# Kernel optimization log

Hardware: AMD Instinct MI355X
Metric: run time of the kernel (lower is better)

## Reference

```python
import jax, jax.numpy as jnp
import numpy as np
import math

H = 8  # num_heads

def _gelu(x):
    return jax.nn.gelu(x, approximate=False)

def setup_inputs() -> dict:
    key = jax.random.key(0)
    ks = jax.random.split(key, 16)
    B, N, T, D = 2, 16, 127, 128
    s = 0.02
    inp = {}
    inp["padded_batches"] = jax.random.normal(ks[0], (B, N, T, D), jnp.float32)
    inp["masks"] = jax.random.randint(ks[1], (B, N, T), 0, 2).astype(jnp.int32)
    inp["positions_3d"] = jax.random.normal(ks[2], (B, N, T, 3), jnp.float32)
    inp["Wq"] = jax.random.normal(ks[3], (D, D), jnp.float32) * s
    inp["bq"] = jnp.zeros((D,), jnp.float32)
    inp["Wk"] = jax.random.normal(ks[4], (D, D), jnp.float32) * s
    inp["bk"] = jnp.zeros((D,), jnp.float32)
    inp["Wv"] = jax.random.normal(ks[5], (D, D), jnp.float32) * s
    inp["bv"] = jnp.zeros((D,), jnp.float32)
    inp["gamma"] = jnp.ones((D,), jnp.float32)
    inp["beta"] = jnp.zeros((D,), jnp.float32)
    inp["token_embedding"] = jax.random.normal(ks[6], (1, D), jnp.float32)
    inp["Wb1"] = jax.random.normal(ks[7], (6, 64), jnp.float32) * s
    inp["bb1"] = jnp.zeros((64,), jnp.float32)
    inp["Wb2"] = jax.random.normal(ks[8], (64, H), jnp.float32) * s
    inp["bb2"] = jnp.zeros((H,), jnp.float32)
    inp["Wv1"] = jax.random.normal(ks[9], (6, 128), jnp.float32) * s
    inp["bv1"] = jnp.zeros((128,), jnp.float32)
    inp["Wv2"] = jax.random.normal(ks[10], (128, D), jnp.float32) * s
    inp["bv2"] = jnp.zeros((D,), jnp.float32)
    return inp

def reference(padded_batches, masks, positions_3d, Wq, bq, Wk, bk, Wv, bv, gamma, beta, token_embedding, Wb1, bb1, Wb2, bb2, Wv1, bv1, Wv2, bv2):
    B, N, T, D = padded_batches.shape
    Hd = D // H
    L = T + 1
    scale = 1.0 / math.sqrt(Hd)
    # prepend cls token
    cls = jnp.broadcast_to(token_embedding, (B, N, 1, D))
    x = jnp.concatenate([cls, padded_batches], axis=-2)  # [B,N,L,D]
    q = (x @ Wq + bq).reshape(B * N, L, H, Hd).transpose(0, 2, 1, 3)
    k = (x @ Wk + bk).reshape(B * N, L, H, Hd).transpose(0, 2, 1, 3)
    v = (x @ Wv + bv).reshape(B * N, L, H, Hd).transpose(0, 2, 1, 3)
    keep = jnp.concatenate([jnp.ones((B, N, 1), masks.dtype), masks], axis=-1)
    large_neg = jnp.finfo(jnp.float32).min
    key_mask = jnp.where(keep == 0, large_neg, 0.0).astype(jnp.float32).reshape(B * N, 1, 1, L)
    logits = jnp.einsum('bhid,bhjd->bhij', q, k) * scale
    # relative positional features
    pos = jnp.concatenate([jnp.zeros((B, N, 1, 3), positions_3d.dtype), positions_3d], axis=-2).reshape(B * N, L, 3)
    diff = pos[:, :, None, :] - pos[:, None, :, :]  # [BN,L,L,3]
    dist2 = jnp.sum(diff ** 2, axis=-1, keepdims=True)
    dist = jnp.sqrt(dist2)
    rel_feat = jnp.concatenate([diff, dist, dist, dist2], axis=-1)  # [BN,L,L,6]
    rel_bias = (_gelu(rel_feat @ Wb1 + bb1) @ Wb2 + bb2).transpose(0, 3, 1, 2)  # [BN,H,L,L]
    rel_bias = rel_bias.at[:, :, 0, :].set(0.0).at[:, :, :, 0].set(0.0)
    logits = logits + rel_bias + key_mask
    w = jax.nn.softmax(logits, axis=-1)
    attn = jnp.einsum('bhij,bhjd->bhid', w, v)
    rel_val = (_gelu(rel_feat @ Wv1 + bv1) @ Wv2 + bv2).reshape(B * N, L, L, H, Hd).transpose(0, 3, 1, 2, 4)
    rel_val = rel_val.at[:, :, 0, :, :].set(0.0).at[:, :, :, 0, :].set(0.0)
    attn = attn + jnp.einsum('bhij,bhijc->bhic', w, rel_val)
    attn = attn.transpose(0, 2, 1, 3).reshape(B, N, L, D)
    st = attn[:, :, :1, :] + x[:, :, :1, :]
    mu = jnp.mean(st, axis=-1, keepdims=True)
    var = jnp.var(st, axis=-1, keepdims=True)
    sum_token = (st - mu) / jnp.sqrt(var + 1e-5) * gamma + beta
    out = attn[:, :, 1:, :] + x[:, :, 1:, :]
    return (out, sum_token)
```

## Files before the change

kernel.cpp:

```cpp
#include <hip/hip_runtime.h>
#include <hip/hip_bf16.h>
#include <math.h>

#define BN 32
#define L 128
#define D 128
#define TT 127
#define NH 8

typedef float f32x4 __attribute__((ext_vector_type(4)));
typedef short s16x8 __attribute__((ext_vector_type(8)));

__device__ __forceinline__ float gelu_sig(float x) {
    float e = __expf(-1.702f * x);
    return x * __builtin_amdgcn_rcpf(1.0f + e);
}
__device__ __forceinline__ unsigned short f2bf(float f) {
    unsigned u = __float_as_uint(f);
    return (unsigned short)((u + 0x7fffu + ((u >> 16) & 1u)) >> 16);
}
__device__ __forceinline__ float bf2f(unsigned short v) {
    return __uint_as_float((unsigned)v << 16);
}

__global__ __launch_bounds__(256)
void qkv_bias_kernel(const float* __restrict__ padded, const float* __restrict__ tok,
                     const float* __restrict__ Wq, const float* __restrict__ bq,
                     const float* __restrict__ Wk, const float* __restrict__ bk,
                     const float* __restrict__ Wv, const float* __restrict__ bv,
                     const float* __restrict__ Wb1, const float* __restrict__ bb1,
                     const float* __restrict__ Wb2, const float* __restrict__ bb2,
                     const float* __restrict__ Wv1, const float* __restrict__ bv1,
                     const float* __restrict__ Wv2,
                     const int* __restrict__ masks, const float* __restrict__ pos3d,
                     float* __restrict__ Qo, float* __restrict__ Ko,
                     unsigned short* __restrict__ VF,
                     float* __restrict__ RVW, unsigned short* __restrict__ WV2F,
                     unsigned short* __restrict__ BIAS) {
    const int bid = blockIdx.x;
    const int tid = threadIdx.x;

    if (bid < 384) {
        const int chunk = bid / 96;
        const int rem = bid % 96;
        const int mat = rem >> 5;
        const int s = rem & 31;
        const float* W = (mat == 0) ? Wq : (mat == 1) ? Wk : Wv;
        const float* bias = (mat == 0) ? bq : (mat == 1) ? bk : bv;
        float* outp = (mat == 0) ? Qo : Ko;

        __shared__ unsigned short Xs[32][136];
        {
            const int row = tid >> 3;
            const int colbase = (tid & 7) * 16;
            const int i = chunk * 32 + row;
            const float* src = (i == 0) ? tok : &padded[(size_t)s * TT * D + (size_t)(i - 1) * D];
#pragma unroll
            for (int k4 = 0; k4 < 4; ++k4) {
                float4 v = *(const float4*)&src[colbase + k4 * 4];
                unsigned lo = (unsigned)f2bf(v.x) | ((unsigned)f2bf(v.y) << 16);
                unsigned hi = (unsigned)f2bf(v.z) | ((unsigned)f2bf(v.w) << 16);
                *(uint2*)&Xs[row][colbase + k4 * 4] = make_uint2(lo, hi);
            }
        }
        __syncthreads();

        const int wave = tid >> 6;
        const int lane = tid & 63;
        const int hA = lane & 15;
        const int kg = lane >> 4;

        s16x8 afr[2][4];
#pragma unroll
        for (int m = 0; m < 2; ++m)
#pragma unroll
            for (int kt = 0; kt < 4; ++kt)
                afr[m][kt] = *(const s16x8*)&Xs[m * 16 + hA][kt * 32 + kg * 8];

        f32x4 acc[2][2];
#pragma unroll
        for (int m = 0; m < 2; ++m)
#pragma unroll
            for (int n = 0; n < 2; ++n) acc[m][n] = (f32x4){0.f, 0.f, 0.f, 0.f};

#pragma unroll
        for (int kt = 0; kt < 4; ++kt) {
#pragma unroll
            for (int n = 0; n < 2; ++n) {
                const int col = (2 * wave + n) * 16 + hA;
                s16x8 bw;
#pragma unroll
                for (int e = 0; e < 8; ++e)
                    bw[e] = (short)f2bf(W[(size_t)(kt * 32 + kg * 8 + e) * D + col]);
                acc[0][n] = __builtin_amdgcn_mfma_f32_16x16x32_bf16(afr[0][kt], bw, acc[0][n], 0, 0, 0);
                acc[1][n] = __builtin_amdgcn_mfma_f32_16x16x32_bf16(afr[1][kt], bw, acc[1][n], 0, 0, 0);
            }
        }

        if (mat != 2) {
#pragma unroll
            for (int n = 0; n < 2; ++n) {
                const int col = (2 * wave + n) * 16 + hA;
                const float bc = bias[col];
#pragma unroll
                for (int m = 0; m < 2; ++m)
#pragma unroll
                    for (int r = 0; r < 4; ++r) {
                        const int row = chunk * 32 + m * 16 + kg * 4 + r;
                        outp[(size_t)s * L * D + (size_t)row * D + col] = acc[m][n][r] + bc;
                    }
            }
        } else {
            __syncthreads();
#pragma unroll
            for (int n = 0; n < 2; ++n) {
                const int col = (2 * wave + n) * 16 + hA;
                const float bc = bias[col];
#pragma unroll
                for (int m = 0; m < 2; ++m)
#pragma unroll
                    for (int r = 0; r < 4; ++r)
                        Xs[m * 16 + kg * 4 + r][col] = f2bf(acc[m][n][r] + bc);
            }
            __syncthreads();
#pragma unroll
            for (int pass = 0; pass < 2; ++pass) {
                const int idx = pass * 256 + tid;
                const int fl = idx >> 6, ln = idx & 63;
                unsigned short v8[8];
#pragma unroll
                for (int e = 0; e < 8; ++e)
                    v8[e] = Xs[(ln >> 4) * 8 + e][fl * 16 + (ln & 15)];
                *(uint4*)&VF[(size_t)s * 16384 + ((size_t)(chunk * 8 + fl) * 64 + ln) * 8] = *(uint4*)v8;
            }
        }

        if (bid == 0) {
            if (tid < 128) {
                const int cc = tid;
                RVW[cc * 8 + 0] = Wv1[0 * 128 + cc];
                RVW[cc * 8 + 1] = Wv1[1 * 128 + cc];
                RVW[cc * 8 + 2] = Wv1[2 * 128 + cc];
                RVW[cc * 8 + 3] = Wv1[3 * 128 + cc] + Wv1[4 * 128 + cc];
                RVW[cc * 8 + 4] = Wv1[5 * 128 + cc];
                RVW[cc * 8 + 5] = bv1[cc];
                RVW[cc * 8 + 6] = 0.f;
                RVW[cc * 8 + 7] = 0.f;
            }
            for (int idx = tid; idx < 16384; idx += 256) {
                int f = idx >> 9, r = idx & 511, ln = r >> 3, e = r & 7;
                int kt = f >> 3, ng = f & 7;
                int row = kt * 32 + (ln >> 4) * 8 + e;
                int col = ng * 16 + (ln & 15);
                WV2F[idx] = f2bf(Wv2[(size_t)row * D + col]);
            }
        }
    } else {
        const int b2 = bid - 384;
        const int s = b2 >> 6;
        const int jp = b2 & 63;
        const int wv = tid >> 6;
        const int lane = tid & 63;
        const int j = jp * 2 + (wv >> 1);
        const int i = (wv & 1) * 64 + lane;

        if (j == 0) return;
        if (!masks[(size_t)s * TT + (j - 1)]) return;
        const float* pj = pos3d + ((size_t)s * TT + (j - 1)) * 3;
        const int im1 = (i > 0) ? (i - 1) : 0;
        const float* pi = pos3d + ((size_t)s * TT + im1) * 3;
        const float pix = (i > 0) ? pi[0] : 0.f;
        const float piy = (i > 0) ? pi[1] : 0.f;
        const float piz = (i > 0) ? pi[2] : 0.f;
        const float dx = pix - pj[0], dy = piy - pj[1], dz = piz - pj[2];
        const float dist2 = dx * dx + dy * dy + dz * dz;
        const float dist = sqrtf(dist2);

        float bias[NH];
#pragma unroll
        for (int hh = 0; hh < NH; ++hh) bias[hh] = 0.f;
#pragma unroll 2
        for (int u = 0; u < 64; ++u) {
            const float w0 = Wb1[u];
            const float w1 = Wb1[64 + u];
            const float w2 = Wb1[128 + u];
            const float w3 = Wb1[192 + u] + Wb1[256 + u];
            const float w4 = Wb1[320 + u];
            float hv = bb1[u];
            hv = fmaf(dx, w0, hv);
            hv = fmaf(dy, w1, hv);
            hv = fmaf(dz, w2, hv);
            hv = fmaf(dist, w3, hv);
            hv = fmaf(dist2, w4, hv);
            hv = gelu_sig(hv);
            const float* w2p = &Wb2[u * 8];
            bias[0] = fmaf(hv, w2p[0], bias[0]);
            bias[1] = fmaf(hv, w2p[1], bias[1]);
            bias[2] = fmaf(hv, w2p[2], bias[2]);
            bias[3] = fmaf(hv, w2p[3], bias[3]);
            bias[4] = fmaf(hv, w2p[4], bias[4]);
            bias[5] = fmaf(hv, w2p[5], bias[5]);
            bias[6] = fmaf(hv, w2p[6], bias[6]);
            bias[7] = fmaf(hv, w2p[7], bias[7]);
        }
        if (i > 0) {
            uint4 ow;
            ow.x = (unsigned)f2bf(bias[0] + bb2[0]) | ((unsigned)f2bf(bias[1] + bb2[1]) << 16);
            ow.y = (unsigned)f2bf(bias[2] + bb2[2]) | ((unsigned)f2bf(bias[3] + bb2[3]) << 16);
            ow.z = (unsigned)f2bf(bias[4] + bb2[4]) | ((unsigned)f2bf(bias[5] + bb2[5]) << 16);
            ow.w = (unsigned)f2bf(bias[6] + bb2[6]) | ((unsigned)f2bf(bias[7] + bb2[7]) << 16);
            *(uint4*)&BIAS[(((size_t)s * L + i) * L + j) * 8] = ow;
        }
    }
}

__global__ __launch_bounds__(256)
void logits_kernel(const float* __restrict__ Q, const float* __restrict__ K,
                   __hip_bfloat16* __restrict__ LW) {
    const int s = blockIdx.x >> 3;
    const int h = blockIdx.x & 7;
    const int tid = threadIdx.x;
    const int wv = tid >> 6;
    const int lane = tid & 63;
    const int lrn = lane & 15;
    const int kg = lane >> 4;

    __shared__ float Qs[128][16];
    __shared__ float Ks[128][16];
    for (int e = tid; e < 2048; e += 256) {
        int i = e >> 4, d = e & 15;
        Qs[i][d] = Q[((size_t)s * L + i) * D + h * 16 + d];
        Ks[i][d] = K[((size_t)s * L + i) * D + h * 16 + d];
    }
    __syncthreads();

    s16x8 afr[2];
#pragma unroll
    for (int m = 0; m < 2; ++m) {
        s16x8 a;
#pragma unroll
        for (int e = 0; e < 8; ++e) a[e] = 0;
        if (kg < 2) {
            const int i = wv * 32 + m * 16 + lrn;
            float4 q0 = *(const float4*)&Qs[i][kg * 8];
            float4 q1 = *(const float4*)&Qs[i][kg * 8 + 4];
            a[0] = (short)f2bf(q0.x); a[1] = (short)f2bf(q0.y);
            a[2] = (short)f2bf(q0.z); a[3] = (short)f2bf(q0.w);
            a[4] = (short)f2bf(q1.x); a[5] = (short)f2bf(q1.y);
            a[6] = (short)f2bf(q1.z); a[7] = (short)f2bf(q1.w);
        }
        afr[m] = a;
    }

    __hip_bfloat16* lw = LW + ((size_t)(s * NH + h) * L) * L;
#pragma unroll
    for (int n = 0; n < 8; ++n) {
        s16x8 b;
#pragma unroll
        for (int e = 0; e < 8; ++e) b[e] = 0;
        if (kg < 2) {
            const int j = n * 16 + lrn;
            float4 k0 = *(const float4*)&Ks[j][kg * 8];
            float4 k1 = *(const float4*)&Ks[j][kg * 8 + 4];
            b[0] = (short)f2bf(k0.x); b[1] = (short)f2bf(k0.y);
            b[2] = (short)f2bf(k0.z); b[3] = (short)f2bf(k0.w);
            b[4] = (short)f2bf(k1.x); b[5] = (short)f2bf(k1.y);
            b[6] = (short)f2bf(k1.z); b[7] = (short)f2bf(k1.w);
        }
#pragma unroll
        for (int m = 0; m < 2; ++m) {
            f32x4 acc = (f32x4){0.f, 0.f, 0.f, 0.f};
            acc = __builtin_amdgcn_mfma_f32_16x16x32_bf16(afr[m], b, acc, 0, 0, 0);
#pragma unroll
            for (int r = 0; r < 4; ++r)
                lw[(size_t)(wv * 32 + m * 16 + kg * 4 + r) * L + n * 16 + lrn] =
                    __float2bfloat16(acc[r] * 0.25f);
        }
    }
}

__global__ __launch_bounds__(256, 4)
void attn_kernel(const float* __restrict__ padded, const int* __restrict__ masks,
                 const float* __restrict__ pos3d,
                 const float* __restrict__ gamma, const float* __restrict__ beta,
                 const float* __restrict__ tok,
                 const float* __restrict__ RVW,
                 const unsigned short* __restrict__ WV2F,
                 const float* __restrict__ bv2,
                 const unsigned short* __restrict__ VF, const __hip_bfloat16* __restrict__ LW,
                 const unsigned short* __restrict__ BIAS,
                 float* __restrict__ out) {
    const int i = blockIdx.x;
    const int s = blockIdx.y;
    const int tid = threadIdx.x;
    const int wave = tid >> 6;
    const int lane = tid & 63;
    const int hA = lane & 15;
    const int kg = lane >> 4;
    const int j = tid & 127;
    const int hbase = (tid >> 7) * 4;

    __shared__ float4 feat4_lds[144];
    __shared__ float  feat5_lds[L];
    __shared__ unsigned short w_bf[NH][136];
    __shared__ unsigned short wu_bf[NH][136];
    __shared__ unsigned short gs_bf[NH][136];
    __shared__ float  a12_lds[2][D];
    __shared__ float  reds[4][NH];
    __shared__ float  red2[2][2];
    __shared__ unsigned long long kb_lds[2];
    __shared__ int    jmap_lds[128];

    __hip_bfloat16 lr4[4];
#pragma unroll
    for (int k = 0; k < 4; ++k)
        lr4[k] = LW[((size_t)(s * NH + hbase + k) * L + i) * L + j];
    const int keep = (j == 0) ? 1 : masks[(size_t)s * TT + (j - 1)];
    const int ub = (i > 0) && (j > 0) && keep;
    uint2 braw = make_uint2(0u, 0u);
    if (ub) braw = *(const uint2*)&BIAS[(((size_t)s * L + i) * L + j) * 8 + hbase];

    const unsigned long long bal = __ballot(keep != 0);
    if (lane == 0 && wave < 2) kb_lds[wave] = bal;

    if (tid < 128) {
        float pix = 0.f, piy = 0.f, piz = 0.f;
        if (i > 0) { const float* pp = pos3d + ((size_t)s * TT + (i - 1)) * 3; pix = pp[0]; piy = pp[1]; piz = pp[2]; }
        float pjx = 0.f, pjy = 0.f, pjz = 0.f;
        if (tid > 0) { const float* pp = pos3d + ((size_t)s * TT + (tid - 1)) * 3; pjx = pp[0]; pjy = pp[1]; pjz = pp[2]; }
        const float dx = pix - pjx, dy = piy - pjy, dz = piz - pjz;
        const float dist2 = dx * dx + dy * dy + dz * dz;
        const float dist = sqrtf(dist2);
        feat4_lds[tid + (tid >> 3)] = make_float4(dx, dy, dz, dist);
        feat5_lds[tid] = dist2;
        jmap_lds[tid] = 0;
    }
    for (int idx = tid; idx < NH * 68; idx += 256) {
        ((unsigned*)w_bf)[idx] = 0u;
        ((unsigned*)wu_bf)[idx] = 0u;
    }
    __syncthreads();

    const unsigned long long b0 = kb_lds[0];
    const int nk = __popcll(b0) + __popcll(kb_lds[1]);
    const int NK32 = (nk + 31) >> 5;
    int rank = 0;
    if (keep) {
        rank = __popcll(bal & ((1ull << lane) - 1)) + ((wave & 1) ? __popcll(b0) : 0);
        if (wave < 2) jmap_lds[rank] = j;
    }

    float badd[4];
    badd[0] = bf2f((unsigned short)(braw.x & 0xffffu));
    badd[1] = bf2f((unsigned short)(braw.x >> 16));
    badd[2] = bf2f((unsigned short)(braw.y & 0xffffu));
    badd[3] = bf2f((unsigned short)(braw.y >> 16));
    float p4[4];
#pragma unroll
    for (int k = 0; k < 4; ++k) {
        float lv = __bfloat162float(lr4[k]) + badd[k];
        p4[k] = keep ? __expf(lv) : 0.f;
    }
#pragma unroll
    for (int k = 0; k < 4; ++k) {
        float v = p4[k];
        for (int off = 32; off >= 1; off >>= 1) v += __shfl_xor(v, off, 64);
        if (lane == 0) reds[wave][hbase + k] = v;
    }
    __syncthreads();
    if (keep) {
        const int pb = (tid >> 7) * 2;
#pragma unroll
        for (int k = 0; k < 4; ++k) {
            const int hh = hbase + k;
            float inv = __builtin_amdgcn_rcpf(reds[pb][hh] + reds[pb + 1][hh]);
            unsigned short wn = f2bf(p4[k] * inv);
            w_bf[hh][rank] = wn;
            wu_bf[hh][j] = wn;
        }
    }
    __syncthreads();

    const int ng0 = 2 * wave;
    const unsigned short* VFs = VF + (size_t)s * 16384;

    f32x4 acc1[2];
    acc1[0] = (f32x4){0.f, 0.f, 0.f, 0.f};
    acc1[1] = (f32x4){0.f, 0.f, 0.f, 0.f};
#pragma unroll
    for (int kt = 0; kt < 4; ++kt) {
        s16x8 wuf;
#pragma unroll
        for (int e = 0; e < 8; ++e) wuf[e] = 0;
        if (hA < NH)
            wuf = *(const s16x8*)&wu_bf[hA][kt * 32 + kg * 8];
#pragma unroll
        for (int n = 0; n < 2; ++n) {
            const int f = kt * 8 + ng0 + n;
            s16x8 bw = *(const s16x8*)&VFs[((size_t)f * 64 + lane) * 8];
            acc1[n] = __builtin_amdgcn_mfma_f32_16x16x32_bf16(wuf, bw, acc1[n], 0, 0, 0);
        }
    }
#pragma unroll
    for (int n = 0; n < 2; ++n) {
        const int f = ng0 + n;
        if (kg == (f >> 2)) a12_lds[0][f * 16 + hA] = acc1[n][f & 3];
    }

    if (i > 0) {
        float rvw[2][6];
#pragma unroll
        for (int n = 0; n < 2; ++n) {
            const int c = (ng0 + n) * 16 + hA;
            float4 ra = *(const float4*)&RVW[(size_t)c * 8 + 0];
            rvw[n][0] = ra.x; rvw[n][1] = ra.y; rvw[n][2] = ra.z; rvw[n][3] = ra.w;
            rvw[n][4] = RVW[(size_t)c * 8 + 4];
            rvw[n][5] = RVW[(size_t)c * 8 + 5];
        }

        f32x4 accG[2];
#pragma unroll
        for (int n = 0; n < 2; ++n) accG[n] = (f32x4){0.f, 0.f, 0.f, 0.f};

#pragma unroll
        for (int kt = 0; kt < 4; ++kt) {
            if (kt >= NK32) break;
            s16x8 wf;
#pragma unroll
            for (int e = 0; e < 8; ++e) wf[e] = 0;
            if (hA < NH) {
                wf = *(const s16x8*)&w_bf[hA][kt * 32 + kg * 8];
                if (kt == 0 && kg == 0) wf[0] = 0;
            }
            s16x8 bfr[2];
#pragma unroll
            for (int e = 0; e < 8; ++e) {
                const int jj = jmap_lds[kt * 32 + kg * 8 + e];
                float4 fa = feat4_lds[jj + (jj >> 3)];
                float f5 = feat5_lds[jj];
#pragma unroll
                for (int n = 0; n < 2; ++n) {
                    float hv = rvw[n][5];
                    hv = fmaf(fa.x, rvw[n][0], hv);
                    hv = fmaf(fa.y, rvw[n][1], hv);
                    hv = fmaf(fa.z, rvw[n][2], hv);
                    hv = fmaf(fa.w, rvw[n][3], hv);
                    hv = fmaf(f5,  rvw[n][4], hv);
                    bfr[n][e] = (short)f2bf(gelu_sig(hv));
                }
            }
#pragma unroll
            for (int n = 0; n < 2; ++n)
                accG[n] = __builtin_amdgcn_mfma_f32_16x16x32_bf16(wf, bfr[n], accG[n], 0, 0, 0);
        }

        if (lane < 32) {
#pragma unroll
            for (int n = 0; n < 2; ++n)
#pragma unroll
                for (int r = 0; r < 4; ++r)
                    gs_bf[(lane >> 4) * 4 + r][(ng0 + n) * 16 + hA] = f2bf(accG[n][r]);
        }
        __syncthreads();

        f32x4 acc2[2];
#pragma unroll
        for (int n = 0; n < 2; ++n) acc2[n] = (f32x4){0.f, 0.f, 0.f, 0.f};
#pragma unroll
        for (int kt = 0; kt < 4; ++kt) {
            s16x8 gf;
#pragma unroll
            for (int e = 0; e < 8; ++e) gf[e] = 0;
            if (hA < NH)
                gf = *(const s16x8*)&gs_bf[hA][kt * 32 + kg * 8];
#pragma unroll
            for (int n = 0; n < 2; ++n) {
                const int f = kt * 8 + ng0 + n;
                s16x8 bw = *(const s16x8*)&WV2F[((size_t)f * 64 + lane) * 8];
                acc2[n] = __builtin_amdgcn_mfma_f32_16x16x32_bf16(gf, bw, acc2[n], 0, 0, 0);
            }
        }
#pragma unroll
        for (int n = 0; n < 2; ++n) {
            const int f = ng0 + n;
            if (kg == (f >> 2)) a12_lds[1][f * 16 + hA] = acc2[n][f & 3];
        }
        __syncthreads();

        if (tid < 128) {
            const float S1 = 1.0f - bf2f(wu_bf[tid >> 4][0]);
            const size_t o = (size_t)s * TT * D + (size_t)(i - 1) * D + tid;
            out[o] = a12_lds[0][tid] + a12_lds[1][tid] + S1 * bv2[tid] + padded[o];
        }
    } else {
        __syncthreads();

        float st = 0.f;
        if (tid < 128) {
            st = a12_lds[0][tid] + tok[tid];
            float sum = st, sum2 = st * st;
            for (int off = 32; off >= 1; off >>= 1) {
                sum += __shfl_xor(sum, off, 64);
                sum2 += __shfl_xor(sum2, off, 64);
            }
            if (lane == 0) { red2[wave][0] = sum; red2[wave][1] = sum2; }
        }
        __syncthreads();
        if (tid < 128) {
            float sum = red2[0][0] + red2[1][0];
            float sum2 = red2[0][1] + red2[1][1];
            const float mu = sum * (1.0f / 128.0f);
            const float var = sum2 * (1.0f / 128.0f) - mu * mu;
            const float y = (st - mu) * rsqrtf(var + 1e-5f) * gamma[tid] + beta[tid];
            out[(size_t)BN * TT * D + (size_t)s * D + tid] = y;
        }
    }
}

extern "C" void kernel_launch(void* const* d_in, const int* in_sizes, int n_in,
                              void* d_out, int out_size, void* d_ws, size_t ws_size,
                              hipStream_t stream) {
    const float* padded = (const float*)d_in[0];
    const int*   masks  = (const int*)d_in[1];
    const float* pos3d  = (const float*)d_in[2];
    const float* Wq = (const float*)d_in[3];
    const float* bq = (const float*)d_in[4];
    const float* Wk = (const float*)d_in[5];
    const float* bk = (const float*)d_in[6];
    const float* Wv = (const float*)d_in[7];
    const float* bv = (const float*)d_in[8];
    const float* gamma = (const float*)d_in[9];
    const float* beta  = (const float*)d_in[10];
    const float* tok   = (const float*)d_in[11];
    const float* Wb1 = (const float*)d_in[12];
    const float* bb1 = (const float*)d_in[13];
    const float* Wb2 = (const float*)d_in[14];
    const float* bb2 = (const float*)d_in[15];
    const float* Wv1 = (const float*)d_in[16];
    const float* bv1 = (const float*)d_in[17];
    const float* Wv2 = (const float*)d_in[18];
    const float* bv2 = (const float*)d_in[19];
    float* out = (float*)d_out;

    float* Q  = (float*)d_ws;
    float* K  = Q + (size_t)BN * L * D;
    unsigned short* VF = (unsigned short*)(K + (size_t)BN * L * D);
    __hip_bfloat16* LW = (__hip_bfloat16*)(VF + (size_t)BN * L * D);
    unsigned short* BIAS = (unsigned short*)(LW + (size_t)BN * NH * L * L);
    float* RVW = (float*)(BIAS + (size_t)BN * L * L * NH);
    unsigned short* WV2F = (unsigned short*)(RVW + 128 * 8);

    qkv_bias_kernel<<<dim3(384 + BN * 64), 256, 0, stream>>>(
        padded, tok, Wq, bq, Wk, bk, Wv, bv, Wb1, bb1, Wb2, bb2, Wv1, bv1, Wv2,
        masks, pos3d, Q, K, VF, RVW, WV2F, BIAS);
    logits_kernel<<<dim3(BN * NH), 256, 0, stream>>>(Q, K, LW);
    attn_kernel<<<dim3(L, BN), 256, 0, stream>>>(padded, masks, pos3d, gamma, beta, tok,
                                                 RVW, WV2F, bv2,
                                                 VF, LW, BIAS, out);
}
```

Before: 76.02 us.

## Fuse QK logits into attention kernel and store K pre-swizzled in bf16

Removes the separate logits kernel and its bf16 logits buffer round trip through global memory. The QKV kernel now writes K in a bf16 MFMA-fragment layout, and each attention block computes its own row of per-head logits with a block-diagonal MFMA using the query row staged in LDS. This saves one launch and the LW write and read. In exchange it adds MFMA work per block, where most of the A operand is zero, plus extra LDS and one more barrier.

```diff
diff --git a/kernel.cpp b/kernel.cpp
--- a/kernel.cpp
+++ b/kernel.cpp
@@ -33,7 +33,7 @@
                      const float* __restrict__ Wv1, const float* __restrict__ bv1,
                      const float* __restrict__ Wv2,
                      const int* __restrict__ masks, const float* __restrict__ pos3d,
-                     float* __restrict__ Qo, float* __restrict__ Ko,
+                     float* __restrict__ Qo, unsigned short* __restrict__ KF,
                      unsigned short* __restrict__ VF,
                      float* __restrict__ RVW, unsigned short* __restrict__ WV2F,
                      unsigned short* __restrict__ BIAS) {
@@ -47,9 +47,8 @@
         const int s = rem & 31;
         const float* W = (mat == 0) ? Wq : (mat == 1) ? Wk : Wv;
         const float* bias = (mat == 0) ? bq : (mat == 1) ? bk : bv;
-        float* outp = (mat == 0) ? Qo : Ko;
-
-        __shared__ unsigned short Xs[32][136];
+
+        __shared__ __align__(16) unsigned short Xs[32][136];
         {
             const int row = tid >> 3;
             const int colbase = (tid & 7) * 16;
@@ -97,7 +96,7 @@
             }
         }
 
-        if (mat != 2) {
+        if (mat == 0) {
 #pragma unroll
             for (int n = 0; n < 2; ++n) {
                 const int col = (2 * wave + n) * 16 + hA;
@@ -107,7 +106,7 @@
 #pragma unroll
                     for (int r = 0; r < 4; ++r) {
                         const int row = chunk * 32 + m * 16 + kg * 4 + r;
-                        outp[(size_t)s * L * D + (size_t)row * D + col] = acc[m][n][r] + bc;
+                        Qo[(size_t)s * L * D + (size_t)row * D + col] = acc[m][n][r] + bc;
                     }
             }
         } else {
@@ -123,15 +122,26 @@
                         Xs[m * 16 + kg * 4 + r][col] = f2bf(acc[m][n][r] + bc);
             }
             __syncthreads();
-#pragma unroll
-            for (int pass = 0; pass < 2; ++pass) {
-                const int idx = pass * 256 + tid;
-                const int fl = idx >> 6, ln = idx & 63;
-                unsigned short v8[8];
-#pragma unroll
-                for (int e = 0; e < 8; ++e)
-                    v8[e] = Xs[(ln >> 4) * 8 + e][fl * 16 + (ln & 15)];
-                *(uint4*)&VF[(size_t)s * 16384 + ((size_t)(chunk * 8 + fl) * 64 + ln) * 8] = *(uint4*)v8;
+            if (mat == 2) {
+#pragma unroll
+                for (int pass = 0; pass < 2; ++pass) {
+                    const int idx = pass * 256 + tid;
+                    const int fl = idx >> 6, ln = idx & 63;
+                    unsigned short v8[8];
+#pragma unroll
+                    for (int e = 0; e < 8; ++e)
+                        v8[e] = Xs[(ln >> 4) * 8 + e][fl * 16 + (ln & 15)];
+                    *(uint4*)&VF[(size_t)s * 16384 + ((size_t)(chunk * 8 + fl) * 64 + ln) * 8] = *(uint4*)v8;
+                }
+            } else {
+#pragma unroll
+                for (int pass = 0; pass < 2; ++pass) {
+                    const int idx = pass * 256 + tid;
+                    const int lf = idx >> 6, ln = idx & 63;
+                    const int kt = lf >> 1, ngl = lf & 1;
+                    uint4 v = *(const uint4*)&Xs[ngl * 16 + (ln & 15)][kt * 32 + (ln >> 4) * 8];
+                    *(uint4*)&KF[(size_t)s * 16384 + ((size_t)(kt * 8 + 2 * chunk + ngl) * 64 + ln) * 8] = v;
+                }
             }
         }
 
@@ -214,71 +224,6 @@
     }
 }
 
-__global__ __launch_bounds__(256)
-void logits_kernel(const float* __restrict__ Q, const float* __restrict__ K,
-                   __hip_bfloat16* __restrict__ LW) {
-    const int s = blockIdx.x >> 3;
-    const int h = blockIdx.x & 7;
-    const int tid = threadIdx.x;
-    const int wv = tid >> 6;
-    const int lane = tid & 63;
-    const int lrn = lane & 15;
-    const int kg = lane >> 4;
-
-    __shared__ float Qs[128][16];
-    __shared__ float Ks[128][16];
-    for (int e = tid; e < 2048; e += 256) {
-        int i = e >> 4, d = e & 15;
-        Qs[i][d] = Q[((size_t)s * L + i) * D + h * 16 + d];
-        Ks[i][d] = K[((size_t)s * L + i) * D + h * 16 + d];
-    }
-    __syncthreads();
-
-    s16x8 afr[2];
-#pragma unroll
-    for (int m = 0; m < 2; ++m) {
-        s16x8 a;
-#pragma unroll
-        for (int e = 0; e < 8; ++e) a[e] = 0;
-        if (kg < 2) {
-            const int i = wv * 32 + m * 16 + lrn;
-            float4 q0 = *(const float4*)&Qs[i][kg * 8];
-            float4 q1 = *(const float4*)&Qs[i][kg * 8 + 4];
-            a[0] = (short)f2bf(q0.x); a[1] = (short)f2bf(q0.y);
-            a[2] = (short)f2bf(q0.z); a[3] = (short)f2bf(q0.w);
-            a[4] = (short)f2bf(q1.x); a[5] = (short)f2bf(q1.y);
-            a[6] = (short)f2bf(q1.z); a[7] = (short)f2bf(q1.w);
-        }
-        afr[m] = a;
-    }
-
-    __hip_bfloat16* lw = LW + ((size_t)(s * NH + h) * L) * L;
-#pragma unroll
-    for (int n = 0; n < 8; ++n) {
-        s16x8 b;
-#pragma unroll
-        for (int e = 0; e < 8; ++e) b[e] = 0;
-        if (kg < 2) {
-            const int j = n * 16 + lrn;
-            float4 k0 = *(const float4*)&Ks[j][kg * 8];
-            float4 k1 = *(const float4*)&Ks[j][kg * 8 + 4];
-            b[0] = (short)f2bf(k0.x); b[1] = (short)f2bf(k0.y);
-            b[2] = (short)f2bf(k0.z); b[3] = (short)f2bf(k0.w);
-            b[4] = (short)f2bf(k1.x); b[5] = (short)f2bf(k1.y);
-            b[6] = (short)f2bf(k1.z); b[7] = (short)f2bf(k1.w);
-        }
-#pragma unroll
-        for (int m = 0; m < 2; ++m) {
-            f32x4 acc = (f32x4){0.f, 0.f, 0.f, 0.f};
-            acc = __builtin_amdgcn_mfma_f32_16x16x32_bf16(afr[m], b, acc, 0, 0, 0);
-#pragma unroll
-            for (int r = 0; r < 4; ++r)
-                lw[(size_t)(wv * 32 + m * 16 + kg * 4 + r) * L + n * 16 + lrn] =
-                    __float2bfloat16(acc[r] * 0.25f);
-        }
-    }
-}
-
 __global__ __launch_bounds__(256, 4)
 void attn_kernel(const float* __restrict__ padded, const int* __restrict__ masks,
                  const float* __restrict__ pos3d,
@@ -287,7 +232,9 @@
                  const float* __restrict__ RVW,
                  const unsigned short* __restrict__ WV2F,
                  const float* __restrict__ bv2,
-                 const unsigned short* __restrict__ VF, const __hip_bfloat16* __restrict__ LW,
+                 const float* __restrict__ Q,
+                 const unsigned short* __restrict__ KF,
+                 const unsigned short* __restrict__ VF,
                  const unsigned short* __restrict__ BIAS,
                  float* __restrict__ out) {
     const int i = blockIdx.x;
@@ -302,6 +249,8 @@
 
     __shared__ float4 feat4_lds[144];
     __shared__ float  feat5_lds[L];
+    __shared__ __align__(16) unsigned short qbf[128];
+    __shared__ float  l_lds[NH][132];
     __shared__ unsigned short w_bf[NH][136];
     __shared__ unsigned short wu_bf[NH][136];
     __shared__ unsigned short gs_bf[NH][136];
@@ -311,10 +260,6 @@
     __shared__ unsigned long long kb_lds[2];
     __shared__ int    jmap_lds[128];
 
-    __hip_bfloat16 lr4[4];
-#pragma unroll
-    for (int k = 0; k < 4; ++k)
-        lr4[k] = LW[((size_t)(s * NH + hbase + k) * L + i) * L + j];
     const int keep = (j == 0) ? 1 : masks[(size_t)s * TT + (j - 1)];
     const int ub = (i > 0) && (j > 0) && keep;
     uint2 braw = make_uint2(0u, 0u);
@@ -324,6 +269,7 @@
     if (lane == 0 && wave < 2) kb_lds[wave] = bal;
 
     if (tid < 128) {
+        qbf[tid] = f2bf(Q[((size_t)s * L + i) * D + tid]);
         float pix = 0.f, piy = 0.f, piz = 0.f;
         if (i > 0) { const float* pp = pos3d + ((size_t)s * TT + (i - 1)) * 3; pix = pp[0]; piy = pp[1]; piz = pp[2]; }
         float pjx = 0.f, pjy = 0.f, pjz = 0.f;
@@ -350,6 +296,38 @@
         if (wave < 2) jmap_lds[rank] = j;
     }
 
+    const int ng0 = 2 * wave;
+    const unsigned short* KFs = KF + (size_t)s * 16384;
+    const unsigned short* VFs = VF + (size_t)s * 16384;
+
+    {
+        f32x4 accL[2];
+        accL[0] = (f32x4){0.f, 0.f, 0.f, 0.f};
+        accL[1] = (f32x4){0.f, 0.f, 0.f, 0.f};
+#pragma unroll
+        for (int kt = 0; kt < 4; ++kt) {
+            const int hslice = kt * 2 + (kg >> 1);
+            s16x8 qa;
+#pragma unroll
+            for (int e = 0; e < 8; ++e) qa[e] = 0;
+            if (hA == hslice)
+                qa = *(const s16x8*)&qbf[kt * 32 + kg * 8];
+#pragma unroll
+            for (int n = 0; n < 2; ++n) {
+                s16x8 bk = *(const s16x8*)&KFs[((size_t)(kt * 8 + ng0 + n) * 64 + lane) * 8];
+                accL[n] = __builtin_amdgcn_mfma_f32_16x16x32_bf16(qa, bk, accL[n], 0, 0, 0);
+            }
+        }
+        if (lane < 32) {
+#pragma unroll
+            for (int n = 0; n < 2; ++n)
+#pragma unroll
+                for (int r = 0; r < 4; ++r)
+                    l_lds[(lane >> 4) * 4 + r][(ng0 + n) * 16 + hA] = accL[n][r];
+        }
+    }
+    __syncthreads();
+
     float badd[4];
     badd[0] = bf2f((unsigned short)(braw.x & 0xffffu));
     badd[1] = bf2f((unsigned short)(braw.x >> 16));
@@ -358,7 +336,7 @@
     float p4[4];
 #pragma unroll
     for (int k = 0; k < 4; ++k) {
-        float lv = __bfloat162float(lr4[k]) + badd[k];
+        float lv = fmaf(l_lds[hbase + k][j], 0.25f, badd[k]);
         p4[k] = keep ? __expf(lv) : 0.f;
     }
 #pragma unroll
@@ -380,9 +358,6 @@
         }
     }
     __syncthreads();
-
-    const int ng0 = 2 * wave;
-    const unsigned short* VFs = VF + (size_t)s * 16384;
 
     f32x4 acc1[2];
     acc1[0] = (f32x4){0.f, 0.f, 0.f, 0.f};
@@ -543,18 +518,16 @@
     float* out = (float*)d_out;
 
     float* Q  = (float*)d_ws;
-    float* K  = Q + (size_t)BN * L * D;
-    unsigned short* VF = (unsigned short*)(K + (size_t)BN * L * D);
-    __hip_bfloat16* LW = (__hip_bfloat16*)(VF + (size_t)BN * L * D);
-    unsigned short* BIAS = (unsigned short*)(LW + (size_t)BN * NH * L * L);
+    unsigned short* KF = (unsigned short*)(Q + (size_t)BN * L * D);
+    unsigned short* VF = KF + (size_t)BN * L * D;
+    unsigned short* BIAS = VF + (size_t)BN * L * D;
     float* RVW = (float*)(BIAS + (size_t)BN * L * L * NH);
     unsigned short* WV2F = (unsigned short*)(RVW + 128 * 8);
 
     qkv_bias_kernel<<<dim3(384 + BN * 64), 256, 0, stream>>>(
         padded, tok, Wq, bq, Wk, bk, Wv, bv, Wb1, bb1, Wb2, bb2, Wv1, bv1, Wv2,
-        masks, pos3d, Q, K, VF, RVW, WV2F, BIAS);
-    logits_kernel<<<dim3(BN * NH), 256, 0, stream>>>(Q, K, LW);
+        masks, pos3d, Q, KF, VF, RVW, WV2F, BIAS);
     attn_kernel<<<dim3(L, BN), 256, 0, stream>>>(padded, masks, pos3d, gamma, beta, tok,
                                                  RVW, WV2F, bv2,
-                                                 VF, LW, BIAS, out);
+                                                 Q, KF, VF, BIAS, out);
 }
```

Measured after the change: 70.28 us. -7.6%, faster.
